# Performance work log

Hardware: AMD Instinct MI355X
Metric: run time of the kernel (lower is better)

The kernel has to match this reference:

```python
import jax, jax.numpy as jnp
import numpy as np

N_NODES = 100000
IN_CH, HID_CH, OUT_CH = 128, 256, 128
N_EDGES = 1600000


def setup_inputs() -> dict:
    key = jax.random.key(0)
    k_x, k_e, k_w1, k_b1, k_w2, k_b2 = jax.random.split(key, 6)
    x = jax.random.normal(k_x, (N_NODES, IN_CH), dtype=jnp.float32)
    edge_index = jax.random.randint(k_e, (2, N_EDGES), 0, N_NODES, dtype=jnp.int64)
    # MLP params (Linear stores weight [out,in]; we keep [in,out] for x @ W)
    lim1 = 1.0 / np.sqrt(IN_CH)
    lim2 = 1.0 / np.sqrt(HID_CH)
    W1 = jax.random.uniform(k_w1, (IN_CH, HID_CH), jnp.float32, -lim1, lim1)
    b1 = jax.random.uniform(k_b1, (HID_CH,), jnp.float32, -lim1, lim1)
    W2 = jax.random.uniform(k_w2, (HID_CH, OUT_CH), jnp.float32, -lim2, lim2)
    b2 = jax.random.uniform(k_b2, (OUT_CH,), jnp.float32, -lim2, lim2)
    eps = jnp.zeros((), jnp.float32)  # train_eps=True, init 0
    return {"x": x, "edge_index": edge_index, "W1": W1, "b1": b1,
            "W2": W2, "b2": b2, "eps": eps}


def reference(x, edge_index, W1, b1, W2, b2, eps):
    src, dst = edge_index[0], edge_index[1]
    # scatter-add neighbor aggregation: aggr[i] = sum_{(j->i)} x[j]
    aggr = jax.ops.segment_sum(x[src], dst, num_segments=N_NODES)  # [N, in]
    h = (1.0 + eps) * x + aggr
    h = jax.nn.relu(h @ W1 + b1)
    h = h @ W2 + b2
    h = jax.nn.relu(h)
    # dropout is identity in eval mode
    return jax.nn.log_softmax(h, axis=-1)
```

## Files before the change

### kernel.cpp

```cpp
#include <hip/hip_runtime.h>

#define N_NODES 100000
#define IN_CH 128
#define HID_CH 256
#define OUT_CH 128
#define N_EDGES 1600000

#define NBK 782
#define BIN_BLOCKS 256
#define EPB (N_EDGES / BIN_BLOCKS)

typedef __attribute__((ext_vector_type(8))) short short8;
typedef __attribute__((ext_vector_type(4))) float f32x4;

__device__ __forceinline__ float b2f(ushort u) {
    unsigned int x = ((unsigned int)u) << 16;
    return __uint_as_float(x);
}
__device__ __forceinline__ ushort f2b(float f) {
    unsigned int u = __float_as_uint(f);
    u += 0x7FFFu + ((u >> 16) & 1u);
    return (ushort)(u >> 16);
}

#define PREP_X_BLOCKS 6250
#define PREP_W1_BLOCKS 128
#define PREP_W2_BLOCKS 128
#define PREP_TOTAL (PREP_X_BLOCKS + PREP_W1_BLOCKS + PREP_W2_BLOCKS)
__global__ __launch_bounds__(256) void prep_kernel(
    const float* __restrict__ x, const float* __restrict__ W1,
    const float* __restrict__ W2, const int* __restrict__ dst,
    ushort* __restrict__ xb, ushort* __restrict__ W1T,
    ushort* __restrict__ W2T, int* __restrict__ histT) {
    const int b = blockIdx.x;
    const int t = threadIdx.x;
    if (b < PREP_X_BLOCKS) {
        const size_t i = (size_t)b * 2048 + t * 8;
        float4 a = *reinterpret_cast<const float4*>(x + i);
        float4 c = *reinterpret_cast<const float4*>(x + i + 4);
        ushort v[8] = {f2b(a.x), f2b(a.y), f2b(a.z), f2b(a.w),
                       f2b(c.x), f2b(c.y), f2b(c.z), f2b(c.w)};
        *reinterpret_cast<short8*>(xb + i) = *reinterpret_cast<short8*>(v);
    } else if (b < PREP_X_BLOCKS + PREP_W1_BLOCKS) {
        const int i = (b - PREP_X_BLOCKS) * 256 + t;
        const int oc = i >> 7, k = i & 127;
        W1T[i] = f2b(W1[k * HID_CH + oc]);
    } else if (b < PREP_TOTAL) {
        const int i = (b - PREP_X_BLOCKS - PREP_W1_BLOCKS) * 256 + t;
        const int oc = i >> 8, k = i & 255;
        W2T[i] = f2b(W2[k * OUT_CH + oc]);
    } else {
        __shared__ int h[NBK];
        const int bb = b - PREP_TOTAL;
        for (int k = t; k < NBK; k += 256) h[k] = 0;
        __syncthreads();
        const int base = bb * EPB;
        for (int i = t; i < EPB; i += 256)
            atomicAdd(&h[dst[base + i] >> 7], 1);
        __syncthreads();
        for (int k = t; k < NBK; k += 256) histT[k * BIN_BLOCKS + bb] = h[k];
    }
}

__global__ __launch_bounds__(256) void scanA_kernel(
    const int* __restrict__ histT, int* __restrict__ blockBaseP,
    int* __restrict__ bktTotal) {
    __shared__ int ts[256];
    const int bk = blockIdx.x, t = threadIdx.x;
    const int v = histT[bk * BIN_BLOCKS + t];
    ts[t] = v;
    __syncthreads();
    #pragma unroll
    for (int o = 1; o < 256; o <<= 1) {
        int add = (t >= o) ? ts[t - o] : 0;
        __syncthreads();
        ts[t] += add;
        __syncthreads();
    }
    blockBaseP[bk * BIN_BLOCKS + t] = ts[t] - v;
    if (t == 255) bktTotal[bk] = ts[255];
}

__global__ __launch_bounds__(1024) void scanB_kernel(
    const int* __restrict__ bktTotal, int* __restrict__ bktBase) {
    __shared__ int ts[1024];
    const int t = threadIdx.x;
    const int v = (t < NBK) ? bktTotal[t] : 0;
    ts[t] = v;
    __syncthreads();
    #pragma unroll
    for (int o = 1; o < 1024; o <<= 1) {
        int add = (t >= o) ? ts[t - o] : 0;
        __syncthreads();
        ts[t] += add;
        __syncthreads();
    }
    if (t < NBK) bktBase[t] = ts[t] - v;
}

__global__ __launch_bounds__(256) void bin_kernel(
    const int* __restrict__ src, const int* __restrict__ dst,
    const int* __restrict__ blockBaseP, const int* __restrict__ bktBase,
    unsigned int* __restrict__ ebuf) {
    __shared__ int base[NBK];
    __shared__ int cur[NBK];
    const int b = blockIdx.x, t = threadIdx.x;
    for (int k = t; k < NBK; k += 256) {
        base[k] = bktBase[k] + blockBaseP[k * BIN_BLOCKS + b];
        cur[k] = 0;
    }
    __syncthreads();
    const int ebase = b * EPB;
    for (int i = t; i < EPB; i += 256) {
        const int d = dst[ebase + i];
        const int s = src[ebase + i];
        const int bk = d >> 7;
        const int r = atomicAdd(&cur[bk], 1);
        ebuf[base[bk] + r] = ((unsigned int)(d & 127) << 17) | (unsigned int)s;
    }
}

__global__ __launch_bounds__(256) void group_kernel(
    const unsigned int* __restrict__ ebuf,
    const int* __restrict__ bktBase, const int* __restrict__ bktTotal,
    int* __restrict__ csr_src, int* __restrict__ offs) {
    __shared__ int hist[128];
    __shared__ int cur[128];
    const int bk = blockIdx.x, t = threadIdx.x;
    if (t < 128) hist[t] = 0;
    __syncthreads();
    const int start = bktBase[bk];
    const int cnt   = bktTotal[bk];
    for (int i = t; i < cnt; i += 256)
        atomicAdd(&hist[ebuf[start + i] >> 17], 1);
    __syncthreads();
    int v = (t < 128) ? hist[t] : 0;
    #pragma unroll
    for (int o = 1; o < 128; o <<= 1) {
        int add = (t < 128 && t >= o) ? hist[t - o] : 0;
        __syncthreads();
        if (t < 128) hist[t] += add;
        __syncthreads();
    }
    if (t < 128) {
        const int excl = hist[t] - v;
        cur[t] = excl;
        const int node = bk * 128 + t;
        if (node < N_NODES) offs[node] = start + excl;
    }
    if (bk == 0 && t == 0) offs[N_NODES] = N_EDGES;
    __syncthreads();
    for (int i = t; i < cnt; i += 256) {
        const unsigned int e = ebuf[start + i];
        const int dl = e >> 17;
        const int p = atomicAdd(&cur[dl], 1);
        csr_src[start + p] = (int)(e & 0x1FFFF);
    }
}

__global__ __launch_bounds__(256) void gather_kernel(
    const ushort* __restrict__ xb,
    const float* __restrict__ eps_p,
    const int* __restrict__ offs,
    const int* __restrict__ csr_src,
    ushort* __restrict__ h_in) {
    const int node = blockIdx.x * 16 + (threadIdx.x >> 4);
    const int l16 = threadIdx.x & 15;
    const int c = l16 * 8;
    const int beg = offs[node];
    const int end = offs[node + 1];

    float a0[8], a1[8], a2[8], a3[8];
    #pragma unroll
    for (int j = 0; j < 8; ++j) { a0[j] = 0.f; a1[j] = 0.f; a2[j] = 0.f; a3[j] = 0.f; }

    for (int base = beg; base < end; base += 16) {
        const int nn = min(16, end - base);
        const int sidx = csr_src[base + min(l16, nn - 1)];
        int i = 0;
        for (; i + 4 <= nn; i += 4) {
            const int s0 = __shfl(sidx, i + 0, 16);
            const int s1 = __shfl(sidx, i + 1, 16);
            const int s2 = __shfl(sidx, i + 2, 16);
            const int s3 = __shfl(sidx, i + 3, 16);
            short8 v0 = *reinterpret_cast<const short8*>(xb + (size_t)s0 * IN_CH + c);
            short8 v1 = *reinterpret_cast<const short8*>(xb + (size_t)s1 * IN_CH + c);
            short8 v2 = *reinterpret_cast<const short8*>(xb + (size_t)s2 * IN_CH + c);
            short8 v3 = *reinterpret_cast<const short8*>(xb + (size_t)s3 * IN_CH + c);
            #pragma unroll
            for (int j = 0; j < 8; ++j) {
                a0[j] += b2f((ushort)v0[j]);
                a1[j] += b2f((ushort)v1[j]);
                a2[j] += b2f((ushort)v2[j]);
                a3[j] += b2f((ushort)v3[j]);
            }
        }
        for (; i < nn; ++i) {
            const int s = __shfl(sidx, i, 16);
            short8 v = *reinterpret_cast<const short8*>(xb + (size_t)s * IN_CH + c);
            #pragma unroll
            for (int j = 0; j < 8; ++j) a0[j] += b2f((ushort)v[j]);
        }
    }

    const float scale = 1.0f + eps_p[0];
    short8 sv = *reinterpret_cast<const short8*>(xb + (size_t)node * IN_CH + c);
    ushort o[8];
    #pragma unroll
    for (int j = 0; j < 8; ++j) {
        const float aggr = (a0[j] + a1[j]) + (a2[j] + a3[j]);
        o[j] = f2b(scale * b2f((ushort)sv[j]) + aggr);
    }
    *reinterpret_cast<short8*>(h_in + (size_t)node * IN_CH + c) =
        *reinterpret_cast<short8*>(o);
}

#define H1_LD 264
__global__ __launch_bounds__(512) void mlp_fused(
    const ushort* __restrict__ h_in,
    const ushort* __restrict__ W1T,
    const ushort* __restrict__ W2T,
    const float* __restrict__ b1,
    const float* __restrict__ b2,
    float* __restrict__ out) {
    __shared__ ushort wbuf[32768];
    __shared__ ushort h1s[8][16 * H1_LD];
    const int t    = threadIdx.x;
    const int w    = t >> 6;
    const int lane = t & 63;
    const int lr   = lane & 15;
    const int lk   = lane >> 4;
    const int row0 = blockIdx.x * 128 + w * 16;
    const int arow = row0 + lr;
    const int arc  = arow < N_NODES ? arow : N_NODES - 1;
    ushort* tile = h1s[w];
    const int sw = (lr & 7) << 3;

    {
        const ushort* gw = W1T + t * 64;
        const int row = t >> 1;
        const int s = (row & 7) << 3;
        ushort* dstp = wbuf + row * 128;
        #pragma unroll
        for (int j = 0; j < 8; ++j) {
            short8 v = *reinterpret_cast<const short8*>(gw + j * 8);
            const int col = (t & 1) * 64 + j * 8;
            *reinterpret_cast<short8*>(dstp + (col ^ s)) = v;
        }
    }

    short8 a[4];
    const ushort* ap = h_in + (size_t)arc * IN_CH + lk * 8;
    #pragma unroll
    for (int kk = 0; kk < 4; ++kk)
        a[kk] = *reinterpret_cast<const short8*>(ap + kk * 32);

    __syncthreads();

    #pragma unroll
    for (int ct = 0; ct < 16; ++ct) {
        const ushort* bp = wbuf + (ct * 16 + lr) * 128;
        f32x4 acc = (f32x4){0.f, 0.f, 0.f, 0.f};
        #pragma unroll
        for (int kk = 0; kk < 4; ++kk) {
            short8 b = *reinterpret_cast<const short8*>(bp + ((lk * 8 + kk * 32) ^ sw));
            acc = __builtin_amdgcn_mfma_f32_16x16x32_bf16(a[kk], b, acc, 0, 0, 0);
        }
        const float bb = b1[ct * 16 + lr];
        #pragma unroll
        for (int r = 0; r < 4; ++r) {
            float v = fmaxf(acc[r] + bb, 0.0f);
            tile[(lk * 4 + r) * H1_LD + ct * 16 + lr] = f2b(v);
        }
    }

    __syncthreads();

    {
        const ushort* gw = W2T + t * 64;
        const int row = t >> 2;
        const int s = (row & 7) << 3;
        ushort* dstp = wbuf + row * 256;
        #pragma unroll
        for (int j = 0; j < 8; ++j) {
            short8 v = *reinterpret_cast<const short8*>(gw + j * 8);
            const int col = (t & 3) * 64 + j * 8;
            *reinterpret_cast<short8*>(dstp + (col ^ s)) = v;
        }
    }

    short8 a2[8];
    #pragma unroll
    for (int kk = 0; kk < 8; ++kk)
        a2[kk] = *reinterpret_cast<const short8*>(tile + lr * H1_LD + lk * 8 + kk * 32);

    __syncthreads();

    f32x4 acc2[8];
    #pragma unroll
    for (int ct = 0; ct < 8; ++ct) acc2[ct] = (f32x4){0.f, 0.f, 0.f, 0.f};

    #pragma unroll
    for (int ct = 0; ct < 8; ++ct) {
        const ushort* bp = wbuf + (ct * 16 + lr) * 256;
        #pragma unroll
        for (int kk = 0; kk < 8; ++kk) {
            short8 b = *reinterpret_cast<const short8*>(bp + ((lk * 8 + kk * 32) ^ sw));
            acc2[ct] = __builtin_amdgcn_mfma_f32_16x16x32_bf16(a2[kk], b, acc2[ct], 0, 0, 0);
        }
    }

    float bias[8];
    #pragma unroll
    for (int ct = 0; ct < 8; ++ct) bias[ct] = b2[ct * 16 + lr];

    const int orow0 = row0 + lk * 4;
    #pragma unroll
    for (int r = 0; r < 4; ++r) {
        float v[8];
        float m = -1e30f;
        #pragma unroll
        for (int ct = 0; ct < 8; ++ct) {
            v[ct] = fmaxf(acc2[ct][r] + bias[ct], 0.0f);
            m = fmaxf(m, v[ct]);
        }
        #pragma unroll
        for (int o = 1; o < 16; o <<= 1) m = fmaxf(m, __shfl_xor(m, o));
        float s = 0.0f;
        #pragma unroll
        for (int ct = 0; ct < 8; ++ct) s += __expf(v[ct] - m);
        #pragma unroll
        for (int o = 1; o < 16; o <<= 1) s += __shfl_xor(s, o);
        const float lse = m + __logf(s);
        const int orow = orow0 + r;
        if (orow < N_NODES) {
            #pragma unroll
            for (int ct = 0; ct < 8; ++ct)
                out[(size_t)orow * OUT_CH + ct * 16 + lr] = v[ct] - lse;
        }
    }
}

extern "C" void kernel_launch(void* const* d_in, const int* in_sizes, int n_in,
                              void* d_out, int out_size, void* d_ws, size_t ws_size,
                              hipStream_t stream) {
    const float* x    = (const float*)d_in[0];
    const int*   ei   = (const int*)d_in[1];
    const float* W1   = (const float*)d_in[2];
    const float* b1   = (const float*)d_in[3];
    const float* W2   = (const float*)d_in[4];
    const float* b2   = (const float*)d_in[5];
    const float* eps  = (const float*)d_in[6];
    float* out = (float*)d_out;

    ushort* xb   = (ushort*)d_ws;
    ushort* h_in = xb + (size_t)N_NODES * IN_CH;
    ushort* W1T  = h_in + (size_t)N_NODES * IN_CH;
    ushort* W2T  = W1T + IN_CH * HID_CH;
    int* histT      = (int*)(W2T + HID_CH * OUT_CH);
    int* blockBaseP = histT + NBK * BIN_BLOCKS;
    int* bktTotal   = blockBaseP + NBK * BIN_BLOCKS;
    int* bktBase    = bktTotal + NBK;
    int* offs       = bktBase + NBK;
    unsigned int* ebuf = (unsigned int*)(offs + N_NODES + 2);
    int* csr_src    = (int*)(ebuf + N_EDGES);

    const int* src = ei;
    const int* dst = ei + N_EDGES;

    prep_kernel<<<PREP_TOTAL + BIN_BLOCKS, 256, 0, stream>>>(
        x, W1, W2, dst, xb, W1T, W2T, histT);
    scanA_kernel<<<NBK, 256, 0, stream>>>(histT, blockBaseP, bktTotal);
    scanB_kernel<<<1, 1024, 0, stream>>>(bktTotal, bktBase);
    bin_kernel<<<BIN_BLOCKS, 256, 0, stream>>>(src, dst, blockBaseP, bktBase, ebuf);
    group_kernel<<<NBK, 256, 0, stream>>>(ebuf, bktBase, bktTotal, csr_src, offs);
    gather_kernel<<<N_NODES / 16, 256, 0, stream>>>(xb, eps, offs, csr_src, h_in);
    mlp_fused<<<(N_NODES + 127) / 128, 512, 0, stream>>>(h_in, W1T, W2T, b1, b2, out);
}
```

Before: 167.7 us.

## Gather each node with a full wavefront split into four edge slices

The gather kernel now assigns one 64-lane wavefront per node instead of 16 lanes. The four 16-lane slices each handle different neighbor edges, then combine their partial sums with cross-slice shuffles. This raises memory-level parallelism per node and removes the serial edge loop within a 16-lane group, aiming to hide gather latency. In exchange it adds a shuffle reduction, and lanes sit idle when a node has fewer than eight edges or in the final store.

```diff
diff --git a/kernel.cpp b/kernel.cpp
--- a/kernel.cpp
+++ b/kernel.cpp
@@ -164,55 +164,64 @@
     const int* __restrict__ offs,
     const int* __restrict__ csr_src,
     ushort* __restrict__ h_in) {
-    const int node = blockIdx.x * 16 + (threadIdx.x >> 4);
-    const int l16 = threadIdx.x & 15;
-    const int c = l16 * 8;
+    const int node = blockIdx.x * 4 + (threadIdx.x >> 6);
+    const int l = threadIdx.x & 63;
+    const int slice = l >> 4;
+    const int c = (l & 15) * 8;
     const int beg = offs[node];
     const int end = offs[node + 1];
 
-    float a0[8], a1[8], a2[8], a3[8];
-    #pragma unroll
-    for (int j = 0; j < 8; ++j) { a0[j] = 0.f; a1[j] = 0.f; a2[j] = 0.f; a3[j] = 0.f; }
-
-    for (int base = beg; base < end; base += 16) {
-        const int nn = min(16, end - base);
-        const int sidx = csr_src[base + min(l16, nn - 1)];
-        int i = 0;
-        for (; i + 4 <= nn; i += 4) {
-            const int s0 = __shfl(sidx, i + 0, 16);
-            const int s1 = __shfl(sidx, i + 1, 16);
-            const int s2 = __shfl(sidx, i + 2, 16);
-            const int s3 = __shfl(sidx, i + 3, 16);
-            short8 v0 = *reinterpret_cast<const short8*>(xb + (size_t)s0 * IN_CH + c);
-            short8 v1 = *reinterpret_cast<const short8*>(xb + (size_t)s1 * IN_CH + c);
-            short8 v2 = *reinterpret_cast<const short8*>(xb + (size_t)s2 * IN_CH + c);
-            short8 v3 = *reinterpret_cast<const short8*>(xb + (size_t)s3 * IN_CH + c);
+    float a0[8], a1[8];
+    #pragma unroll
+    for (int j = 0; j < 8; ++j) { a0[j] = 0.f; a1[j] = 0.f; }
+
+    int base = beg;
+    for (; base + 8 <= end; base += 8) {
+        const int sidx = csr_src[base + (l & 7)];
+        const int sA = __shfl(sidx, slice, 64);
+        const int sB = __shfl(sidx, 4 + slice, 64);
+        short8 vA = *reinterpret_cast<const short8*>(xb + (size_t)sA * IN_CH + c);
+        short8 vB = *reinterpret_cast<const short8*>(xb + (size_t)sB * IN_CH + c);
+        #pragma unroll
+        for (int j = 0; j < 8; ++j) {
+            a0[j] += b2f((ushort)vA[j]);
+            a1[j] += b2f((ushort)vB[j]);
+        }
+    }
+    const int r = end - base;
+    if (r > 0) {
+        const int sidx = csr_src[base + min(l & 7, r - 1)];
+        const int sA = __shfl(sidx, min(slice, r - 1), 64);
+        const int sB = __shfl(sidx, min(4 + slice, r - 1), 64);
+        if (slice < r) {
+            short8 vA = *reinterpret_cast<const short8*>(xb + (size_t)sA * IN_CH + c);
             #pragma unroll
-            for (int j = 0; j < 8; ++j) {
-                a0[j] += b2f((ushort)v0[j]);
-                a1[j] += b2f((ushort)v1[j]);
-                a2[j] += b2f((ushort)v2[j]);
-                a3[j] += b2f((ushort)v3[j]);
-            }
-        }
-        for (; i < nn; ++i) {
-            const int s = __shfl(sidx, i, 16);
-            short8 v = *reinterpret_cast<const short8*>(xb + (size_t)s * IN_CH + c);
+            for (int j = 0; j < 8; ++j) a0[j] += b2f((ushort)vA[j]);
+        }
+        if (4 + slice < r) {
+            short8 vB = *reinterpret_cast<const short8*>(xb + (size_t)sB * IN_CH + c);
             #pragma unroll
-            for (int j = 0; j < 8; ++j) a0[j] += b2f((ushort)v[j]);
-        }
-    }
-
-    const float scale = 1.0f + eps_p[0];
-    short8 sv = *reinterpret_cast<const short8*>(xb + (size_t)node * IN_CH + c);
-    ushort o[8];
+            for (int j = 0; j < 8; ++j) a1[j] += b2f((ushort)vB[j]);
+        }
+    }
+
     #pragma unroll
     for (int j = 0; j < 8; ++j) {
-        const float aggr = (a0[j] + a1[j]) + (a2[j] + a3[j]);
-        o[j] = f2b(scale * b2f((ushort)sv[j]) + aggr);
-    }
-    *reinterpret_cast<short8*>(h_in + (size_t)node * IN_CH + c) =
-        *reinterpret_cast<short8*>(o);
+        a0[j] += a1[j];
+        a0[j] += __shfl_xor(a0[j], 16, 64);
+        a0[j] += __shfl_xor(a0[j], 32, 64);
+    }
+
+    if (l < 16) {
+        const float scale = 1.0f + eps_p[0];
+        short8 sv = *reinterpret_cast<const short8*>(xb + (size_t)node * IN_CH + c);
+        ushort o[8];
+        #pragma unroll
+        for (int j = 0; j < 8; ++j)
+            o[j] = f2b(scale * b2f((ushort)sv[j]) + a0[j]);
+        *reinterpret_cast<short8*>(h_in + (size_t)node * IN_CH + c) =
+            *reinterpret_cast<short8*>(o);
+    }
 }
 
 #define H1_LD 264
@@ -374,6 +383,6 @@
     scanB_kernel<<<1, 1024, 0, stream>>>(bktTotal, bktBase);
     bin_kernel<<<BIN_BLOCKS, 256, 0, stream>>>(src, dst, blockBaseP, bktBase, ebuf);
     group_kernel<<<NBK, 256, 0, stream>>>(ebuf, bktBase, bktTotal, csr_src, offs);
-    gather_kernel<<<N_NODES / 16, 256, 0, stream>>>(xb, eps, offs, csr_src, h_in);
+    gather_kernel<<<N_NODES / 4, 256, 0, stream>>>(xb, eps, offs, csr_src, h_in);
     mlp_fused<<<(N_NODES + 127) / 128, 512, 0, stream>>>(h_in, W1T, W2T, b1, b2, out);
 }
```

Result: no change. 169.6 us (+1.1%).
